# Kernel tuning notes

Measured on AMD Instinct MI355X. Metric: run time of the kernel, lower is better.

Reference implementation:

```python
import jax, jax.numpy as jnp
import numpy as np

B, T, N, E = 64, 500, 21, 210
IN_DIM, HID, OUT_DIM = 1, 128, 1


def gcn_norm(edge_index, edge_weight, num_nodes):
    # PyG gcn_norm: add self loops (weight 1), deg over target nodes, symmetric normalization.
    src, dst = edge_index[0], edge_index[1]
    loop = jnp.arange(num_nodes)
    src = jnp.concatenate([src, loop])
    dst = jnp.concatenate([dst, loop])
    ew = jnp.concatenate([edge_weight, jnp.ones((num_nodes,), edge_weight.dtype)])
    deg = jnp.zeros((num_nodes,), edge_weight.dtype).at[dst].add(ew)
    dinv = jnp.where(deg > 0, deg ** -0.5, 0.0)
    norm = dinv[src] * ew * dinv[dst]
    # Dense N x N (N=21, tiny) normalized adjacency; out[i] = sum_j A[i, j] x[j].
    return jnp.zeros((num_nodes, num_nodes), edge_weight.dtype).at[dst, src].add(norm)


def _forward(edge_index, x, edge_weight, Wz_1, bz_1, lzw_1, lzb_1, Wr_1, br_1, lrw_1, lrb_1, Wh_1, bh_1, lhw_1, lhb_1, Wz_2, bz_2, lzw_2, lzb_2, Wr_2, br_2, lrw_2, lrb_2, Wh_2, bh_2, lhw_2, lhb_2, cls_w, cls_b):
    A = gcn_norm(edge_index, edge_weight, N)

    def gcn(X, W, b):  # X: (B, N, F)
        return jnp.einsum("ij,bjf->bif", A, X @ W) + b

    def cell(X, H, Wz, bz, lzw, lzb, Wr, br, lrw, lrb, Wh, bh, lhw, lhb):
        Z = jax.nn.sigmoid(jnp.concatenate([gcn(X, Wz, bz), H], -1) @ lzw + lzb)
        R = jax.nn.sigmoid(jnp.concatenate([gcn(X, Wr, br), H], -1) @ lrw + lrb)
        Ht = jnp.tanh(jnp.concatenate([gcn(X, Wh, bh), H * R], -1) @ lhw + lhb)
        return Z * H + (1.0 - Z) * Ht

    def step(carry, x_t):  # x_t: (B, N)
        H1, H2 = carry
        X = x_t[..., None]  # (B, N, 1)
        H1 = cell(X, H1, Wz_1, bz_1, lzw_1, lzb_1, Wr_1, br_1, lrw_1, lrb_1, Wh_1, bh_1, lhw_1, lhb_1)
        H2 = cell(H1, H2, Wz_2, bz_2, lzw_2, lzb_2, Wr_2, br_2, lrw_2, lrb_2, Wh_2, bh_2, lhw_2, lhb_2)
        return (H1, H2), H2.mean(axis=1)  # mean over nodes -> (B, HID)

    H0 = jnp.zeros((x.shape[0], N, HID), x.dtype)
    _, outs = jax.lax.scan(step, (H0, H0), jnp.moveaxis(x, 1, 0))  # outs: (T, B, HID)
    seq_out = outs.mean(axis=0)  # mean over time (== mean over nodes then time in original)
    return seq_out @ cls_w + cls_b  # (B, OUT_DIM)


def setup_inputs():
    key = jax.random.key(0)
    ks = list(jax.random.split(key, 20))
    kit = iter(ks)

    def nrm(shape, scale=0.05):
        return jax.random.normal(next(kit), shape, jnp.float32) * scale

    inp = {}
    inp["x"] = jax.random.normal(next(kit), (B, T, N), jnp.float32)
    inp["edge_index"] = jax.random.randint(next(kit), (2, E), 0, N)
    inp["edge_weight"] = jax.random.uniform(next(kit), (E,), jnp.float32)
    for tag, in_dim in (("1", IN_DIM), ("2", HID)):
        for g in "zrh":
            inp[f"W{g}_{tag}"] = nrm((in_dim, HID))
            inp[f"b{g}_{tag}"] = jnp.zeros((HID,), jnp.float32)
            inp[f"l{g}w_{tag}"] = nrm((2 * HID, HID))
            inp[f"l{g}b_{tag}"] = jnp.zeros((HID,), jnp.float32)
    inp["cls_w"] = nrm((HID, OUT_DIM))
    inp["cls_b"] = jnp.zeros((OUT_DIM,), jnp.float32)
    return inp


def reference(x, edge_index, edge_weight, Wz_1, bz_1, lzw_1, lzb_1, Wr_1, br_1, lrw_1, lrb_1, Wh_1, bh_1, lhw_1, lhb_1, Wz_2, bz_2, lzw_2, lzb_2, Wr_2, br_2, lrw_2, lrb_2, Wh_2, bh_2, lhw_2, lhb_2, cls_w, cls_b):
    return _forward(edge_index, x, edge_weight, Wz_1, bz_1, lzw_1, lzb_1, Wr_1, br_1, lrw_1, lrb_1, Wh_1, bh_1, lhw_1, lhb_1, Wz_2, bz_2, lzw_2, lzb_2, Wr_2, br_2, lrw_2, lrb_2, Wh_2, bh_2, lhw_2, lhb_2, cls_w, cls_b)
```

## Files before the change

kernel.cpp:

```cpp
#include <hip/hip_runtime.h>
#include <hip/hip_bf16.h>


#define NN 21
#define NROW 24
#define HID 128
#define TSTEPS 500
#define EDGES 210
#define NTHREADS 512
#define RPT 6

#define WS_A     0
#define WS_VEC   1600
#define WS_LZR1  3200
#define WS_LH1   36000
#define WS_WE2   52400
#define WS_LZR2  101600
#define WS_LH2   134400

#define WAVE_SYNC() asm volatile("s_waitcnt lgkmcnt(0)" ::: "memory")

typedef float v2f __attribute__((ext_vector_type(2)));

__device__ __forceinline__ v2f lo2(float4 w) { v2f v = {w.x, w.y}; return v; }
__device__ __forceinline__ v2f hi2(float4 w) { v2f v = {w.z, w.w}; return v; }
__device__ __forceinline__ void pkf(v2f& acc, float s, v2f w) {
    v2f ss = {s, s};
    acc = __builtin_elementwise_fma(ss, w, acc);
}
__device__ __forceinline__ float sigmoidf(float v) {
    return 1.0f / (1.0f + expf(-v));
}

__global__ void build_A(const int* __restrict__ ei, const float* __restrict__ ew,
                        float* __restrict__ Aout) {
    __shared__ double deg[NN];
    __shared__ double dinv[NN];
    __shared__ double Asm[NN * NN];
    int t = threadIdx.x;
    for (int k = t; k < NN * NN; k += blockDim.x) Asm[k] = 0.0;
    if (t < NN) deg[t] = 1.0;
    __syncthreads();
    if (t == 0) {
        for (int e = 0; e < EDGES; e++) deg[ei[EDGES + e]] += (double)ew[e];
        for (int i = 0; i < NN; i++) dinv[i] = deg[i] > 0.0 ? 1.0 / sqrt(deg[i]) : 0.0;
        for (int e = 0; e < EDGES; e++) {
            int s = ei[e], d = ei[EDGES + e];
            Asm[d * NN + s] += dinv[s] * (double)ew[e] * dinv[d];
        }
        for (int i = 0; i < NN; i++) Asm[i * NN + i] += dinv[i] * dinv[i];
    }
    __syncthreads();
    for (int k = t; k < NROW * NN; k += blockDim.x)
        Aout[k] = (k < NN * NN) ? (float)Asm[k] : 0.0f;
}

__global__ void pack_bot(const float* __restrict__ w0, const float* __restrict__ w1,
                         float4* __restrict__ out, int ngate) {
    int t = blockIdx.x * blockDim.x + threadIdx.x;
    int per_c = ngate * 128;
    int total = 32 * per_c;
    if (t >= total) return;
    int c = t / per_c, rem = t - c * per_c;
    int gate = rem >> 7;
    int r2 = rem & 127;
    int k2 = r2 >> 6;
    int f0 = r2 & 63;
    int k = 4 * c + 2 * k2;
    const float* src = (gate == 0) ? w0 : w1;
    float4 v;
    v.x = src[(128 + k) * 128 + f0];
    v.y = src[(128 + k) * 128 + f0 + 64];
    v.z = src[(128 + k + 1) * 128 + f0];
    v.w = src[(128 + k + 1) * 128 + f0 + 64];
    out[t] = v;
}

__global__ void make_weff2(const float* __restrict__ Wz2, const float* __restrict__ Wr2,
                           const float* __restrict__ Wh2,
                           const float* __restrict__ lzw2, const float* __restrict__ lrw2,
                           const float* __restrict__ lhw2,
                           float4* __restrict__ out) {
    int t = blockIdx.x * blockDim.x + threadIdx.x;
    if (t >= 32 * 384) return;
    int c = t / 384, rem = t - c * 384;
    int g = rem >> 7;
    int r2 = rem & 127;
    int k2 = r2 >> 6;
    int f0 = r2 & 63;
    int k = 4 * c + 2 * k2;
    const float* W = (g == 0) ? Wz2 : (g == 1) ? Wr2 : Wh2;
    const float* L = (g == 0) ? lzw2 : (g == 1) ? lrw2 : lhw2;
    double a0 = 0, a1 = 0, a2 = 0, a3 = 0;
    for (int m = 0; m < 128; m++) {
        double w0 = (double)W[k * 128 + m];
        double w1 = (double)W[(k + 1) * 128 + m];
        a0 += w0 * (double)L[m * 128 + f0];
        a1 += w0 * (double)L[m * 128 + f0 + 64];
        a2 += w1 * (double)L[m * 128 + f0];
        a3 += w1 * (double)L[m * 128 + f0 + 64];
    }
    out[t] = make_float4((float)a0, (float)a1, (float)a2, (float)a3);
}

__global__ void make_vecs(const float* __restrict__ Wz1, const float* __restrict__ Wr1,
                          const float* __restrict__ Wh1,
                          const float* __restrict__ bz1, const float* __restrict__ br1,
                          const float* __restrict__ bh1,
                          const float* __restrict__ lzw1, const float* __restrict__ lrw1,
                          const float* __restrict__ lhw1,
                          const float* __restrict__ lzb1, const float* __restrict__ lrb1,
                          const float* __restrict__ lhb1,
                          const float* __restrict__ bz2, const float* __restrict__ br2,
                          const float* __restrict__ bh2,
                          const float* __restrict__ lzw2, const float* __restrict__ lrw2,
                          const float* __restrict__ lhw2,
                          const float* __restrict__ lzb2, const float* __restrict__ lrb2,
                          const float* __restrict__ lhb2,
                          float* __restrict__ out) {
    int t = blockIdx.x * blockDim.x + threadIdx.x;
    if (t >= 9 * 128) return;
    int v = t >> 7, f = t & 127;
    double acc = 0.0;
    if (v < 3) {
        const float* W = (v == 0) ? Wz1 : (v == 1) ? Wr1 : Wh1;
        const float* L = (v == 0) ? lzw1 : (v == 1) ? lrw1 : lhw1;
        for (int m = 0; m < 128; m++) acc += (double)W[m] * (double)L[m * 128 + f];
    } else if (v < 6) {
        int g = v - 3;
        const float* bb = (g == 0) ? bz1 : (g == 1) ? br1 : bh1;
        const float* L  = (g == 0) ? lzw1 : (g == 1) ? lrw1 : lhw1;
        const float* lb = (g == 0) ? lzb1 : (g == 1) ? lrb1 : lhb1;
        for (int m = 0; m < 128; m++) acc += (double)bb[m] * (double)L[m * 128 + f];
        acc += (double)lb[f];
    } else {
        int g = v - 6;
        const float* bb = (g == 0) ? bz2 : (g == 1) ? br2 : bh2;
        const float* L  = (g == 0) ? lzw2 : (g == 1) ? lrw2 : lhw2;
        const float* lb = (g == 0) ? lzb2 : (g == 1) ? lrb2 : lhb2;
        for (int m = 0; m < 128; m++) acc += (double)bb[m] * (double)L[m * 128 + f];
        acc += (double)lb[f];
    }
    out[t] = (float)acc;
}

__global__ __launch_bounds__(NTHREADS, 2) void tgcn_main(
    const float* __restrict__ x,
    const float* __restrict__ ws,
    const float* __restrict__ cls_w,
    const float* __restrict__ cls_b,
    float* __restrict__ out)
{
    const int b  = blockIdx.x;
    const int t  = threadIdx.x;
    const bool isA = (t < 256);
    const int lt = t & 255;
    const int f0 = lt & 63;
    const int f1 = f0 + 64;
    const int gw = __builtin_amdgcn_readfirstlane(lt >> 6);
    const int iA = gw * RPT;
    const int nreal = (iA + RPT <= NN) ? RPT : (NN - iA);

    __shared__ __align__(16) float sH1[2][NROW * HID];
    __shared__ __align__(16) float sH2[NROW * HID];
    __shared__ __align__(16) float sHR1[NROW * HID];
    __shared__ __align__(16) float sHR2[NROW * HID];
    __shared__ __align__(16) float sAH[NROW * HID];
    __shared__ float sA[NROW * NN];
    __shared__ float sax[2][NROW];
    __shared__ double sred[4][HID];

    const float*  vecs = ws + WS_VEC;
    const float4* Lzr1 = (const float4*)(ws + WS_LZR1);
    const float4* Lh1  = (const float4*)(ws + WS_LH1);
    const float4* We2  = (const float4*)(ws + WS_WE2);
    const float4* Lzr2 = (const float4*)(ws + WS_LZR2);
    const float4* Lh2  = (const float4*)(ws + WS_LH2);

    const float4* H2v  = (const float4*)sH2;
    const float4* HR1v = (const float4*)sHR1;
    const float4* HR2v = (const float4*)sHR2;
    const float4* AHv  = (const float4*)sAH;

    for (int k = t; k < 2 * NROW * HID; k += NTHREADS) ((float*)sH1)[k] = 0.0f;
    for (int k = t; k < NROW * HID; k += NTHREADS) sH2[k] = 0.0f;
    for (int k = t; k < NROW * NN; k += NTHREADS) sA[k] = ws[WS_A + k];

    const v2f wz1v = {vecs[f0],        vecs[f1]};
    const v2f wr1v = {vecs[128 + f0],  vecs[128 + f1]};
    const v2f wh1v = {vecs[256 + f0],  vecs[256 + f1]};
    const v2f cz1v = {vecs[384 + f0],  vecs[384 + f1]};
    const v2f cr1v = {vecs[512 + f0],  vecs[512 + f1]};
    const v2f ch1v = {vecs[640 + f0],  vecs[640 + f1]};
    const v2f cz2v = {vecs[768 + f0],  vecs[768 + f1]};
    const v2f cr2v = {vecs[896 + f0],  vecs[896 + f1]};
    const v2f ch2v = {vecs[1024 + f0], vecs[1024 + f1]};

    __syncthreads();

    const float* xb = x + (size_t)b * (TSTEPS * NN);
    if (t < NROW) {
        float a0s = 0.0f, a1s = 0.0f;
        for (int j = 0; j < NN; j++) {
            a0s = fmaf(sA[t * NN + j], xb[j], a0s);
            a1s = fmaf(sA[t * NN + j], xb[NN + j], a1s);
        }
        sax[0][t] = a0s;
        sax[1][t] = a1s;
    }
    __syncthreads();

    double oacc0 = 0.0, oacc1 = 0.0;

    auto layer1 = [&](int s) {
        const float* H1rd = sH1[(s + 1) & 1];
        float*       H1wr = sH1[s & 1];
        const float4* H1c = (const float4*)H1rd;
        float axp[RPT];
        #pragma unroll
        for (int r = 0; r < RPT; r++) axp[r] = sax[s & 1][iA + r];
        v2f az[RPT], ar[RPT];
        #pragma unroll
        for (int r = 0; r < RPT; r++) {
            az[r] = __builtin_elementwise_fma((v2f){axp[r], axp[r]}, wz1v, cz1v);
            ar[r] = __builtin_elementwise_fma((v2f){axp[r], axp[r]}, wr1v, cr1v);
        }
        #pragma unroll 2
        for (int c = 0; c < 32; ++c) {
            const float4 wz0 = Lzr1[c * 256 + f0];
            const float4 wz1 = Lzr1[c * 256 + 64 + f0];
            const float4 wr0 = Lzr1[c * 256 + 128 + f0];
            const float4 wr1 = Lzr1[c * 256 + 192 + f0];
            #pragma unroll
            for (int r = 0; r < RPT; r++) {
                const float4 h = H1c[(iA + r) * 32 + c];
                pkf(az[r], h.x, lo2(wz0)); pkf(az[r], h.y, hi2(wz0));
                pkf(az[r], h.z, lo2(wz1)); pkf(az[r], h.w, hi2(wz1));
                pkf(ar[r], h.x, lo2(wr0)); pkf(ar[r], h.y, hi2(wr0));
                pkf(ar[r], h.z, lo2(wr1)); pkf(ar[r], h.w, hi2(wr1));
            }
        }
        v2f zg[RPT], h1c[RPT];
        #pragma unroll
        for (int r = 0; r < RPT; r++) {
            zg[r].x = sigmoidf(az[r].x);
            zg[r].y = sigmoidf(az[r].y);
            const float r0 = sigmoidf(ar[r].x);
            const float r1 = sigmoidf(ar[r].y);
            h1c[r].x = H1rd[(iA + r) * HID + f0];
            h1c[r].y = H1rd[(iA + r) * HID + f1];
            sHR1[(iA + r) * HID + f0] = h1c[r].x * r0;
            sHR1[(iA + r) * HID + f1] = h1c[r].y * r1;
        }
        WAVE_SYNC();
        v2f ah[RPT];
        #pragma unroll
        for (int r = 0; r < RPT; r++)
            ah[r] = __builtin_elementwise_fma((v2f){axp[r], axp[r]}, wh1v, ch1v);
        #pragma unroll 2
        for (int c = 0; c < 32; ++c) {
            const float4 wh0 = Lh1[c * 128 + f0];
            const float4 wh1 = Lh1[c * 128 + 64 + f0];
            #pragma unroll
            for (int r = 0; r < RPT; r++) {
                const float4 q = HR1v[(iA + r) * 32 + c];
                pkf(ah[r], q.x, lo2(wh0)); pkf(ah[r], q.y, hi2(wh0));
                pkf(ah[r], q.z, lo2(wh1)); pkf(ah[r], q.w, hi2(wh1));
            }
        }
        #pragma unroll
        for (int r = 0; r < RPT; r++) {
            const float n0 = fmaf(zg[r].x, h1c[r].x, (1.0f - zg[r].x) * tanhf(ah[r].x));
            const float n1 = fmaf(zg[r].y, h1c[r].y, (1.0f - zg[r].y) * tanhf(ah[r].y));
            H1wr[(iA + r) * HID + f0] = n0;
            H1wr[(iA + r) * HID + f1] = n1;
        }
    };

    if (isA) layer1(0);
    __syncthreads();

    for (int k = 0; k < TSTEPS; k++) {
        if (isA) {
            if (k + 1 < TSTEPS) {
                layer1(k + 1);
                if (t < NROW && k + 2 < TSTEPS) {
                    const float* xt = xb + (size_t)(k + 2) * NN;
                    float a = 0.0f;
                    for (int j = 0; j < NN; j++) a = fmaf(sA[t * NN + j], xt[j], a);
                    sax[(k + 2) & 1][t] = a;
                }
            }
        } else {
            const float* H1rd = sH1[k & 1];
            v2f aa[RPT];
            #pragma unroll
            for (int r = 0; r < RPT; r++) aa[r] = (v2f){0.0f, 0.0f};
            #pragma unroll 3
            for (int j = 0; j < NN; j++) {
                const v2f hj = {H1rd[j * HID + f0], H1rd[j * HID + f1]};
                #pragma unroll
                for (int r = 0; r < RPT; r++) {
                    const float arj = sA[(iA + r) * NN + j];
                    acc_p3: ;
                    aa[r] = __builtin_elementwise_fma((v2f){arj, arj}, hj, aa[r]);
                }
            }
            #pragma unroll
            for (int r = 0; r < RPT; r++) {
                sAH[(iA + r) * HID + f0] = aa[r].x;
                sAH[(iA + r) * HID + f1] = aa[r].y;
            }
            WAVE_SYNC();
            v2f pz[RPT], pr[RPT], ph[RPT];
            #pragma unroll
            for (int r = 0; r < RPT; r++) { pz[r] = cz2v; pr[r] = cr2v; ph[r] = ch2v; }
            for (int c = 0; c < 32; ++c) {
                const float4 wz0 = We2[c * 384 + f0];
                const float4 wz1 = We2[c * 384 + 64 + f0];
                const float4 wr0 = We2[c * 384 + 128 + f0];
                const float4 wr1 = We2[c * 384 + 192 + f0];
                const float4 wh0 = We2[c * 384 + 256 + f0];
                const float4 wh1 = We2[c * 384 + 320 + f0];
                const float4 lz0 = Lzr2[c * 256 + f0];
                const float4 lz1 = Lzr2[c * 256 + 64 + f0];
                const float4 lr0 = Lzr2[c * 256 + 128 + f0];
                const float4 lr1 = Lzr2[c * 256 + 192 + f0];
                #pragma unroll
                for (int r = 0; r < RPT; r++) {
                    const float4 a = AHv[(iA + r) * 32 + c];
                    const float4 q = H2v[(iA + r) * 32 + c];
                    pkf(pz[r], a.x, lo2(wz0)); pkf(pz[r], a.y, hi2(wz0));
                    pkf(pz[r], a.z, lo2(wz1)); pkf(pz[r], a.w, hi2(wz1));
                    pkf(pz[r], q.x, lo2(lz0)); pkf(pz[r], q.y, hi2(lz0));
                    pkf(pz[r], q.z, lo2(lz1)); pkf(pz[r], q.w, hi2(lz1));
                    pkf(pr[r], a.x, lo2(wr0)); pkf(pr[r], a.y, hi2(wr0));
                    pkf(pr[r], a.z, lo2(wr1)); pkf(pr[r], a.w, hi2(wr1));
                    pkf(pr[r], q.x, lo2(lr0)); pkf(pr[r], q.y, hi2(lr0));
                    pkf(pr[r], q.z, lo2(lr1)); pkf(pr[r], q.w, hi2(lr1));
                    pkf(ph[r], a.x, lo2(wh0)); pkf(ph[r], a.y, hi2(wh0));
                    pkf(ph[r], a.z, lo2(wh1)); pkf(ph[r], a.w, hi2(wh1));
                }
            }
            v2f z2[RPT], h2c[RPT];
            #pragma unroll
            for (int r = 0; r < RPT; r++) {
                z2[r].x = sigmoidf(pz[r].x);
                z2[r].y = sigmoidf(pz[r].y);
                const float r20 = sigmoidf(pr[r].x);
                const float r21 = sigmoidf(pr[r].y);
                h2c[r].x = sH2[(iA + r) * HID + f0];
                h2c[r].y = sH2[(iA + r) * HID + f1];
                sHR2[(iA + r) * HID + f0] = h2c[r].x * r20;
                sHR2[(iA + r) * HID + f1] = h2c[r].y * r21;
            }
            WAVE_SYNC();
            #pragma unroll 2
            for (int c = 0; c < 32; ++c) {
                const float4 lh0 = Lh2[c * 128 + f0];
                const float4 lh1 = Lh2[c * 128 + 64 + f0];
                #pragma unroll
                for (int r = 0; r < RPT; r++) {
                    const float4 q = HR2v[(iA + r) * 32 + c];
                    pkf(ph[r], q.x, lo2(lh0)); pkf(ph[r], q.y, hi2(lh0));
                    pkf(ph[r], q.z, lo2(lh1)); pkf(ph[r], q.w, hi2(lh1));
                }
            }
            #pragma unroll
            for (int r = 0; r < RPT; r++) {
                const float m0 = fmaf(z2[r].x, h2c[r].x, (1.0f - z2[r].x) * tanhf(ph[r].x));
                const float m1 = fmaf(z2[r].y, h2c[r].y, (1.0f - z2[r].y) * tanhf(ph[r].y));
                sH2[(iA + r) * HID + f0] = m0;
                sH2[(iA + r) * HID + f1] = m1;
                if (r < nreal) {
                    oacc0 += (double)m0;
                    oacc1 += (double)m1;
                }
            }
        }
        __syncthreads();
    }

    if (!isA) {
        sred[gw][f0] = oacc0;
        sred[gw][f1] = oacc1;
    }
    __syncthreads();
    if (t < HID) {
        double s = 0.0;
        for (int gg = 0; gg < 4; gg++) s += sred[gg][t];
        sred[0][t] = (s / (double)(TSTEPS * NN)) * (double)cls_w[t];
    }
    __syncthreads();
    if (t < 64) {
        double v = ((double*)sred)[t] + ((double*)sred)[t + 64];
        for (int off = 32; off; off >>= 1) v += __shfl_down(v, off, 64);
        if (t == 0) out[b] = (float)(v + (double)cls_b[0]);
    }
}

extern "C" void kernel_launch(void* const* d_in, const int* in_sizes, int n_in,
                              void* d_out, int out_size, void* d_ws, size_t ws_size,
                              hipStream_t stream) {
    const float* x    = (const float*)d_in[0];
    const int*   ei   = (const int*)  d_in[1];
    const float* ew   = (const float*)d_in[2];
    const float* Wz1  = (const float*)d_in[3];
    const float* bz1  = (const float*)d_in[4];
    const float* lzw1 = (const float*)d_in[5];
    const float* lzb1 = (const float*)d_in[6];
    const float* Wr1  = (const float*)d_in[7];
    const float* br1  = (const float*)d_in[8];
    const float* lrw1 = (const float*)d_in[9];
    const float* lrb1 = (const float*)d_in[10];
    const float* Wh1  = (const float*)d_in[11];
    const float* bh1  = (const float*)d_in[12];
    const float* lhw1 = (const float*)d_in[13];
    const float* lhb1 = (const float*)d_in[14];
    const float* Wz2  = (const float*)d_in[15];
    const float* bz2  = (const float*)d_in[16];
    const float* lzw2 = (const float*)d_in[17];
    const float* lzb2 = (const float*)d_in[18];
    const float* Wr2  = (const float*)d_in[19];
    const float* br2  = (const float*)d_in[20];
    const float* lrw2 = (const float*)d_in[21];
    const float* lrb2 = (const float*)d_in[22];
    const float* Wh2  = (const float*)d_in[23];
    const float* bh2  = (const float*)d_in[24];
    const float* lhw2 = (const float*)d_in[25];
    const float* lhb2 = (const float*)d_in[26];
    const float* clsw = (const float*)d_in[27];
    const float* clsb = (const float*)d_in[28];

    float* ws   = (float*)d_ws;
    float* outp = (float*)d_out;

    build_A<<<1, 64, 0, stream>>>(ei, ew, ws + WS_A);
    pack_bot<<<32, 256, 0, stream>>>(lzw1, lrw1, (float4*)(ws + WS_LZR1), 2);
    pack_bot<<<16, 256, 0, stream>>>(lhw1, lhw1, (float4*)(ws + WS_LH1), 1);
    pack_bot<<<32, 256, 0, stream>>>(lzw2, lrw2, (float4*)(ws + WS_LZR2), 2);
    pack_bot<<<16, 256, 0, stream>>>(lhw2, lhw2, (float4*)(ws + WS_LH2), 1);
    make_weff2<<<48, 256, 0, stream>>>(Wz2, Wr2, Wh2, lzw2, lrw2, lhw2,
                                       (float4*)(ws + WS_WE2));
    make_vecs<<<5, 256, 0, stream>>>(Wz1, Wr1, Wh1, bz1, br1, bh1,
                                     lzw1, lrw1, lhw1, lzb1, lrb1, lhb1,
                                     bz2, br2, bh2, lzw2, lrw2, lhw2,
                                     lzb2, lrb2, lhb2, ws + WS_VEC);
    tgcn_main<<<64, NTHREADS, 0, stream>>>(x, ws, clsw, clsb, outp);
}
```

Baseline: 12.50 ms.

## Remap lanes across rows and columns, pad LDS rows, replace wave syncs with barriers

Each wave now owns a 16-column slice across all row blocks, not one row block across all 64 columns. The 16 lanes within a row group read weight float4s, so each global or L2 weight load is shared by fewer rows per wave but spread differently. The LDS row stride is padded to 132 floats to avoid bank conflicts. Because a wave's outputs are now read by other waves, the intra-wave lgkmcnt syncs are replaced by block-wide __syncthreads, and each step is split into three phases. Loop unroll pragmas are dropped. This adds two extra block barriers per timestep and changes register pressure.

```diff
diff --git a/kernel.cpp b/kernel.cpp
--- a/kernel.cpp
+++ b/kernel.cpp
@@ -9,6 +9,8 @@
 #define EDGES 210
 #define NTHREADS 512
 #define RPT 6
+#define RS 132
+#define RS4 33
 
 #define WS_A     0
 #define WS_VEC   1600
@@ -17,8 +19,6 @@
 #define WS_WE2   52400
 #define WS_LZR2  101600
 #define WS_LH2   134400
-
-#define WAVE_SYNC() asm volatile("s_waitcnt lgkmcnt(0)" ::: "memory")
 
 typedef float v2f __attribute__((ext_vector_type(2)));
 
@@ -151,21 +151,24 @@
     const float* __restrict__ cls_b,
     float* __restrict__ out)
 {
-    const int b  = blockIdx.x;
-    const int t  = threadIdx.x;
+    const int b    = blockIdx.x;
+    const int t    = threadIdx.x;
     const bool isA = (t < 256);
-    const int lt = t & 255;
-    const int f0 = lt & 63;
-    const int f1 = f0 + 64;
-    const int gw = __builtin_amdgcn_readfirstlane(lt >> 6);
-    const int iA = gw * RPT;
+    const int lt   = t & 255;
+    const int w    = __builtin_amdgcn_readfirstlane(lt >> 6);
+    const int lane = lt & 63;
+    const int cp   = lane & 15;
+    const int rb   = lane >> 4;
+    const int f0   = w * 16 + cp;
+    const int f1   = f0 + 64;
+    const int iA   = rb * RPT;
     const int nreal = (iA + RPT <= NN) ? RPT : (NN - iA);
 
-    __shared__ __align__(16) float sH1[2][NROW * HID];
-    __shared__ __align__(16) float sH2[NROW * HID];
-    __shared__ __align__(16) float sHR1[NROW * HID];
-    __shared__ __align__(16) float sHR2[NROW * HID];
-    __shared__ __align__(16) float sAH[NROW * HID];
+    __shared__ __align__(16) float sH1[2][NROW * RS];
+    __shared__ __align__(16) float sH2[NROW * RS];
+    __shared__ __align__(16) float sHR1[NROW * RS];
+    __shared__ __align__(16) float sHR2[NROW * RS];
+    __shared__ __align__(16) float sAH[NROW * RS];
     __shared__ float sA[NROW * NN];
     __shared__ float sax[2][NROW];
     __shared__ double sred[4][HID];
@@ -182,8 +185,8 @@
     const float4* HR2v = (const float4*)sHR2;
     const float4* AHv  = (const float4*)sAH;
 
-    for (int k = t; k < 2 * NROW * HID; k += NTHREADS) ((float*)sH1)[k] = 0.0f;
-    for (int k = t; k < NROW * HID; k += NTHREADS) sH2[k] = 0.0f;
+    for (int k = t; k < 2 * NROW * RS; k += NTHREADS) ((float*)sH1)[k] = 0.0f;
+    for (int k = t; k < NROW * RS; k += NTHREADS) sH2[k] = 0.0f;
     for (int k = t; k < NROW * NN; k += NTHREADS) sA[k] = ws[WS_A + k];
 
     const v2f wz1v = {vecs[f0],        vecs[f1]};
@@ -212,20 +215,21 @@
 
     double oacc0 = 0.0, oacc1 = 0.0;
 
-    auto layer1 = [&](int s) {
+    float axpA[RPT];
+    v2f   zgA[RPT], h1cA[RPT];
+    v2f   phB[RPT], z2B[RPT], h2cB[RPT];
+
+    auto a_p1 = [&](int s) {
         const float* H1rd = sH1[(s + 1) & 1];
-        float*       H1wr = sH1[s & 1];
         const float4* H1c = (const float4*)H1rd;
-        float axp[RPT];
         #pragma unroll
-        for (int r = 0; r < RPT; r++) axp[r] = sax[s & 1][iA + r];
+        for (int r = 0; r < RPT; r++) axpA[r] = sax[s & 1][iA + r];
         v2f az[RPT], ar[RPT];
         #pragma unroll
         for (int r = 0; r < RPT; r++) {
-            az[r] = __builtin_elementwise_fma((v2f){axp[r], axp[r]}, wz1v, cz1v);
-            ar[r] = __builtin_elementwise_fma((v2f){axp[r], axp[r]}, wr1v, cr1v);
-        }
-        #pragma unroll 2
+            az[r] = __builtin_elementwise_fma((v2f){axpA[r], axpA[r]}, wz1v, cz1v);
+            ar[r] = __builtin_elementwise_fma((v2f){axpA[r], axpA[r]}, wr1v, cr1v);
+        }
         for (int c = 0; c < 32; ++c) {
             const float4 wz0 = Lzr1[c * 256 + f0];
             const float4 wz1 = Lzr1[c * 256 + 64 + f0];
@@ -233,88 +237,86 @@
             const float4 wr1 = Lzr1[c * 256 + 192 + f0];
             #pragma unroll
             for (int r = 0; r < RPT; r++) {
-                const float4 h = H1c[(iA + r) * 32 + c];
+                const float4 h = H1c[(iA + r) * RS4 + c];
                 pkf(az[r], h.x, lo2(wz0)); pkf(az[r], h.y, hi2(wz0));
                 pkf(az[r], h.z, lo2(wz1)); pkf(az[r], h.w, hi2(wz1));
                 pkf(ar[r], h.x, lo2(wr0)); pkf(ar[r], h.y, hi2(wr0));
                 pkf(ar[r], h.z, lo2(wr1)); pkf(ar[r], h.w, hi2(wr1));
             }
         }
-        v2f zg[RPT], h1c[RPT];
         #pragma unroll
         for (int r = 0; r < RPT; r++) {
-            zg[r].x = sigmoidf(az[r].x);
-            zg[r].y = sigmoidf(az[r].y);
+            zgA[r].x = sigmoidf(az[r].x);
+            zgA[r].y = sigmoidf(az[r].y);
             const float r0 = sigmoidf(ar[r].x);
             const float r1 = sigmoidf(ar[r].y);
-            h1c[r].x = H1rd[(iA + r) * HID + f0];
-            h1c[r].y = H1rd[(iA + r) * HID + f1];
-            sHR1[(iA + r) * HID + f0] = h1c[r].x * r0;
-            sHR1[(iA + r) * HID + f1] = h1c[r].y * r1;
-        }
-        WAVE_SYNC();
+            h1cA[r].x = H1rd[(iA + r) * RS + f0];
+            h1cA[r].y = H1rd[(iA + r) * RS + f1];
+            sHR1[(iA + r) * RS + f0] = h1cA[r].x * r0;
+            sHR1[(iA + r) * RS + f1] = h1cA[r].y * r1;
+        }
+    };
+    auto a_p2 = [&](int s) {
+        float* H1wr = sH1[s & 1];
         v2f ah[RPT];
         #pragma unroll
         for (int r = 0; r < RPT; r++)
-            ah[r] = __builtin_elementwise_fma((v2f){axp[r], axp[r]}, wh1v, ch1v);
-        #pragma unroll 2
+            ah[r] = __builtin_elementwise_fma((v2f){axpA[r], axpA[r]}, wh1v, ch1v);
         for (int c = 0; c < 32; ++c) {
             const float4 wh0 = Lh1[c * 128 + f0];
             const float4 wh1 = Lh1[c * 128 + 64 + f0];
             #pragma unroll
             for (int r = 0; r < RPT; r++) {
-                const float4 q = HR1v[(iA + r) * 32 + c];
+                const float4 q = HR1v[(iA + r) * RS4 + c];
                 pkf(ah[r], q.x, lo2(wh0)); pkf(ah[r], q.y, hi2(wh0));
                 pkf(ah[r], q.z, lo2(wh1)); pkf(ah[r], q.w, hi2(wh1));
             }
         }
         #pragma unroll
         for (int r = 0; r < RPT; r++) {
-            const float n0 = fmaf(zg[r].x, h1c[r].x, (1.0f - zg[r].x) * tanhf(ah[r].x));
-            const float n1 = fmaf(zg[r].y, h1c[r].y, (1.0f - zg[r].y) * tanhf(ah[r].y));
-            H1wr[(iA + r) * HID + f0] = n0;
-            H1wr[(iA + r) * HID + f1] = n1;
+            const float n0 = fmaf(zgA[r].x, h1cA[r].x, (1.0f - zgA[r].x) * tanhf(ah[r].x));
+            const float n1 = fmaf(zgA[r].y, h1cA[r].y, (1.0f - zgA[r].y) * tanhf(ah[r].y));
+            H1wr[(iA + r) * RS + f0] = n0;
+            H1wr[(iA + r) * RS + f1] = n1;
         }
     };
 
-    if (isA) layer1(0);
+    if (isA) a_p1(0);
+    __syncthreads();
+    if (isA) a_p2(0);
     __syncthreads();
 
     for (int k = 0; k < TSTEPS; k++) {
+        const bool doA = (k + 1 < TSTEPS);
         if (isA) {
-            if (k + 1 < TSTEPS) {
-                layer1(k + 1);
-                if (t < NROW && k + 2 < TSTEPS) {
-                    const float* xt = xb + (size_t)(k + 2) * NN;
-                    float a = 0.0f;
-                    for (int j = 0; j < NN; j++) a = fmaf(sA[t * NN + j], xt[j], a);
-                    sax[(k + 2) & 1][t] = a;
-                }
-            }
+            if (doA) a_p1(k + 1);
         } else {
             const float* H1rd = sH1[k & 1];
             v2f aa[RPT];
             #pragma unroll
             for (int r = 0; r < RPT; r++) aa[r] = (v2f){0.0f, 0.0f};
-            #pragma unroll 3
             for (int j = 0; j < NN; j++) {
-                const v2f hj = {H1rd[j * HID + f0], H1rd[j * HID + f1]};
+                const v2f hj = {H1rd[j * RS + f0], H1rd[j * RS + f1]};
                 #pragma unroll
                 for (int r = 0; r < RPT; r++) {
                     const float arj = sA[(iA + r) * NN + j];
-                    acc_p3: ;
                     aa[r] = __builtin_elementwise_fma((v2f){arj, arj}, hj, aa[r]);
                 }
             }
             #pragma unroll
             for (int r = 0; r < RPT; r++) {
-                sAH[(iA + r) * HID + f0] = aa[r].x;
-                sAH[(iA + r) * HID + f1] = aa[r].y;
-            }
-            WAVE_SYNC();
-            v2f pz[RPT], pr[RPT], ph[RPT];
-            #pragma unroll
-            for (int r = 0; r < RPT; r++) { pz[r] = cz2v; pr[r] = cr2v; ph[r] = ch2v; }
+                sAH[(iA + r) * RS + f0] = aa[r].x;
+                sAH[(iA + r) * RS + f1] = aa[r].y;
+            }
+        }
+        __syncthreads();
+
+        if (isA) {
+            if (doA) a_p2(k + 1);
+        } else {
+            v2f pz[RPT], pr[RPT];
+            #pragma unroll
+            for (int r = 0; r < RPT; r++) { pz[r] = cz2v; pr[r] = cr2v; phB[r] = ch2v; }
             for (int c = 0; c < 32; ++c) {
                 const float4 wz0 = We2[c * 384 + f0];
                 const float4 wz1 = We2[c * 384 + 64 + f0];
@@ -328,8 +330,8 @@
                 const float4 lr1 = Lzr2[c * 256 + 192 + f0];
                 #pragma unroll
                 for (int r = 0; r < RPT; r++) {
-                    const float4 a = AHv[(iA + r) * 32 + c];
-                    const float4 q = H2v[(iA + r) * 32 + c];
+                    const float4 a = AHv[(iA + r) * RS4 + c];
+                    const float4 q = H2v[(iA + r) * RS4 + c];
                     pkf(pz[r], a.x, lo2(wz0)); pkf(pz[r], a.y, hi2(wz0));
                     pkf(pz[r], a.z, lo2(wz1)); pkf(pz[r], a.w, hi2(wz1));
                     pkf(pz[r], q.x, lo2(lz0)); pkf(pz[r], q.y, hi2(lz0));
@@ -338,40 +340,48 @@
                     pkf(pr[r], a.z, lo2(wr1)); pkf(pr[r], a.w, hi2(wr1));
                     pkf(pr[r], q.x, lo2(lr0)); pkf(pr[r], q.y, hi2(lr0));
                     pkf(pr[r], q.z, lo2(lr1)); pkf(pr[r], q.w, hi2(lr1));
-                    pkf(ph[r], a.x, lo2(wh0)); pkf(ph[r], a.y, hi2(wh0));
-                    pkf(ph[r], a.z, lo2(wh1)); pkf(ph[r], a.w, hi2(wh1));
+                    pkf(phB[r], a.x, lo2(wh0)); pkf(phB[r], a.y, hi2(wh0));
+                    pkf(phB[r], a.z, lo2(wh1)); pkf(phB[r], a.w, hi2(wh1));
                 }
             }
-            v2f z2[RPT], h2c[RPT];
             #pragma unroll
             for (int r = 0; r < RPT; r++) {
-                z2[r].x = sigmoidf(pz[r].x);
-                z2[r].y = sigmoidf(pz[r].y);
+                z2B[r].x = sigmoidf(pz[r].x);
+                z2B[r].y = sigmoidf(pz[r].y);
                 const float r20 = sigmoidf(pr[r].x);
                 const float r21 = sigmoidf(pr[r].y);
-                h2c[r].x = sH2[(iA + r) * HID + f0];
-                h2c[r].y = sH2[(iA + r) * HID + f1];
-                sHR2[(iA + r) * HID + f0] = h2c[r].x * r20;
-                sHR2[(iA + r) * HID + f1] = h2c[r].y * r21;
-            }
-            WAVE_SYNC();
-            #pragma unroll 2
+                h2cB[r].x = sH2[(iA + r) * RS + f0];
+                h2cB[r].y = sH2[(iA + r) * RS + f1];
+                sHR2[(iA + r) * RS + f0] = h2cB[r].x * r20;
+                sHR2[(iA + r) * RS + f1] = h2cB[r].y * r21;
+            }
+        }
+        __syncthreads();
+
+        if (isA) {
+            if (t < NROW && k + 2 < TSTEPS) {
+                const float* xt = xb + (size_t)(k + 2) * NN;
+                float a = 0.0f;
+                for (int j = 0; j < NN; j++) a = fmaf(sA[t * NN + j], xt[j], a);
+                sax[(k + 2) & 1][t] = a;
+            }
+        } else {
             for (int c = 0; c < 32; ++c) {
                 const float4 lh0 = Lh2[c * 128 + f0];
                 const float4 lh1 = Lh2[c * 128 + 64 + f0];
                 #pragma unroll
                 for (int r = 0; r < RPT; r++) {
-                    const float4 q = HR2v[(iA + r) * 32 + c];
-                    pkf(ph[r], q.x, lo2(lh0)); pkf(ph[r], q.y, hi2(lh0));
-                    pkf(ph[r], q.z, lo2(lh1)); pkf(ph[r], q.w, hi2(lh1));
+                    const float4 q = HR2v[(iA + r) * RS4 + c];
+                    pkf(phB[r], q.x, lo2(lh0)); pkf(phB[r], q.y, hi2(lh0));
+                    pkf(phB[r], q.z, lo2(lh1)); pkf(phB[r], q.w, hi2(lh1));
                 }
             }
             #pragma unroll
             for (int r = 0; r < RPT; r++) {
-                const float m0 = fmaf(z2[r].x, h2c[r].x, (1.0f - z2[r].x) * tanhf(ph[r].x));
-                const float m1 = fmaf(z2[r].y, h2c[r].y, (1.0f - z2[r].y) * tanhf(ph[r].y));
-                sH2[(iA + r) * HID + f0] = m0;
-                sH2[(iA + r) * HID + f1] = m1;
+                const float m0 = fmaf(z2B[r].x, h2cB[r].x, (1.0f - z2B[r].x) * tanhf(phB[r].x));
+                const float m1 = fmaf(z2B[r].y, h2cB[r].y, (1.0f - z2B[r].y) * tanhf(phB[r].y));
+                sH2[(iA + r) * RS + f0] = m0;
+                sH2[(iA + r) * RS + f1] = m1;
                 if (r < nreal) {
                     oacc0 += (double)m0;
                     oacc1 += (double)m1;
@@ -382,8 +392,8 @@
     }
 
     if (!isA) {
-        sred[gw][f0] = oacc0;
-        sred[gw][f1] = oacc1;
+        sred[rb][f0] = oacc0;
+        sred[rb][f1] = oacc1;
     }
     __syncthreads();
     if (t < HID) {
```

Result: slower. 16.76 ms (+34.1%).

## Move hidden-state and A·H operand reads from LDS to global memory buffers

Applied to the files above, without the earlier changes.

Moves the H1 read buffer, the A·H1 product and H2 out of shared memory into per-block global workspace, read through float4 global loads. Each thread keeps its own previous hidden values in registers, so the gate update no longer reloads them. The aim is to relieve LDS bandwidth and bank pressure by sending matmul operand reads through the vector cache. It removes a wave-level sync after the A·H write and drops several unroll pragmas. The cost is global-memory latency on the critical recurrence and a dependence on the cache staying coherent for data written and then read within the same block.

```diff
diff --git a/kernel.cpp b/kernel.cpp
--- a/kernel.cpp
+++ b/kernel.cpp
@@ -17,6 +17,9 @@
 #define WS_WE2   52400
 #define WS_LZR2  101600
 #define WS_LH2   134400
+#define WS_H1G   150784
+#define WS_AHG   544000
+#define WS_H2G   740608
 
 #define WAVE_SYNC() asm volatile("s_waitcnt lgkmcnt(0)" ::: "memory")
 
@@ -147,6 +150,9 @@
 __global__ __launch_bounds__(NTHREADS, 2) void tgcn_main(
     const float* __restrict__ x,
     const float* __restrict__ ws,
+    float* __restrict__ h1g,
+    float* __restrict__ ahg,
+    float* __restrict__ h2g,
     const float* __restrict__ cls_w,
     const float* __restrict__ cls_b,
     float* __restrict__ out)
@@ -161,11 +167,13 @@
     const int iA = gw * RPT;
     const int nreal = (iA + RPT <= NN) ? RPT : (NN - iA);
 
+    float* h1gb = h1g + (size_t)b * 6144;
+    float* ahgb = ahg + (size_t)b * 3072;
+    float* h2gb = h2g + (size_t)b * 3072;
+
     __shared__ __align__(16) float sH1[2][NROW * HID];
-    __shared__ __align__(16) float sH2[NROW * HID];
     __shared__ __align__(16) float sHR1[NROW * HID];
     __shared__ __align__(16) float sHR2[NROW * HID];
-    __shared__ __align__(16) float sAH[NROW * HID];
     __shared__ float sA[NROW * NN];
     __shared__ float sax[2][NROW];
     __shared__ double sred[4][HID];
@@ -177,13 +185,12 @@
     const float4* Lzr2 = (const float4*)(ws + WS_LZR2);
     const float4* Lh2  = (const float4*)(ws + WS_LH2);
 
-    const float4* H2v  = (const float4*)sH2;
     const float4* HR1v = (const float4*)sHR1;
     const float4* HR2v = (const float4*)sHR2;
-    const float4* AHv  = (const float4*)sAH;
 
     for (int k = t; k < 2 * NROW * HID; k += NTHREADS) ((float*)sH1)[k] = 0.0f;
-    for (int k = t; k < NROW * HID; k += NTHREADS) sH2[k] = 0.0f;
+    for (int k = t; k < 6144; k += NTHREADS) h1gb[k] = 0.0f;
+    for (int k = t; k < 3072; k += NTHREADS) h2gb[k] = 0.0f;
     for (int k = t; k < NROW * NN; k += NTHREADS) sA[k] = ws[WS_A + k];
 
     const v2f wz1v = {vecs[f0],        vecs[f1]};
@@ -212,10 +219,15 @@
 
     double oacc0 = 0.0, oacc1 = 0.0;
 
+    v2f h1keep[RPT];
+    v2f h2keep[RPT];
+    #pragma unroll
+    for (int r = 0; r < RPT; r++) { h1keep[r] = (v2f){0.f, 0.f}; h2keep[r] = (v2f){0.f, 0.f}; }
+
     auto layer1 = [&](int s) {
-        const float* H1rd = sH1[(s + 1) & 1];
-        float*       H1wr = sH1[s & 1];
-        const float4* H1c = (const float4*)H1rd;
+        const float4* gH1 = (const float4*)(h1gb + ((s + 1) & 1) * 3072);
+        float* H1wrL = sH1[s & 1];
+        float* H1wrG = h1gb + (s & 1) * 3072;
         float axp[RPT];
         #pragma unroll
         for (int r = 0; r < RPT; r++) axp[r] = sax[s & 1][iA + r];
@@ -225,7 +237,6 @@
             az[r] = __builtin_elementwise_fma((v2f){axp[r], axp[r]}, wz1v, cz1v);
             ar[r] = __builtin_elementwise_fma((v2f){axp[r], axp[r]}, wr1v, cr1v);
         }
-        #pragma unroll 2
         for (int c = 0; c < 32; ++c) {
             const float4 wz0 = Lzr1[c * 256 + f0];
             const float4 wz1 = Lzr1[c * 256 + 64 + f0];
@@ -233,7 +244,7 @@
             const float4 wr1 = Lzr1[c * 256 + 192 + f0];
             #pragma unroll
             for (int r = 0; r < RPT; r++) {
-                const float4 h = H1c[(iA + r) * 32 + c];
+                const float4 h = gH1[(iA + r) * 32 + c];
                 pkf(az[r], h.x, lo2(wz0)); pkf(az[r], h.y, hi2(wz0));
                 pkf(az[r], h.z, lo2(wz1)); pkf(az[r], h.w, hi2(wz1));
                 pkf(ar[r], h.x, lo2(wr0)); pkf(ar[r], h.y, hi2(wr0));
@@ -247,8 +258,7 @@
             zg[r].y = sigmoidf(az[r].y);
             const float r0 = sigmoidf(ar[r].x);
             const float r1 = sigmoidf(ar[r].y);
-            h1c[r].x = H1rd[(iA + r) * HID + f0];
-            h1c[r].y = H1rd[(iA + r) * HID + f1];
+            h1c[r] = h1keep[r];
             sHR1[(iA + r) * HID + f0] = h1c[r].x * r0;
             sHR1[(iA + r) * HID + f1] = h1c[r].y * r1;
         }
@@ -257,7 +267,6 @@
         #pragma unroll
         for (int r = 0; r < RPT; r++)
             ah[r] = __builtin_elementwise_fma((v2f){axp[r], axp[r]}, wh1v, ch1v);
-        #pragma unroll 2
         for (int c = 0; c < 32; ++c) {
             const float4 wh0 = Lh1[c * 128 + f0];
             const float4 wh1 = Lh1[c * 128 + 64 + f0];
@@ -272,8 +281,11 @@
         for (int r = 0; r < RPT; r++) {
             const float n0 = fmaf(zg[r].x, h1c[r].x, (1.0f - zg[r].x) * tanhf(ah[r].x));
             const float n1 = fmaf(zg[r].y, h1c[r].y, (1.0f - zg[r].y) * tanhf(ah[r].y));
-            H1wr[(iA + r) * HID + f0] = n0;
-            H1wr[(iA + r) * HID + f1] = n1;
+            H1wrL[(iA + r) * HID + f0] = n0;
+            H1wrL[(iA + r) * HID + f1] = n1;
+            H1wrG[(iA + r) * HID + f0] = n0;
+            H1wrG[(iA + r) * HID + f1] = n1;
+            h1keep[r] = (v2f){n0, n1};
         }
     };
 
@@ -296,22 +308,21 @@
             v2f aa[RPT];
             #pragma unroll
             for (int r = 0; r < RPT; r++) aa[r] = (v2f){0.0f, 0.0f};
-            #pragma unroll 3
             for (int j = 0; j < NN; j++) {
                 const v2f hj = {H1rd[j * HID + f0], H1rd[j * HID + f1]};
                 #pragma unroll
                 for (int r = 0; r < RPT; r++) {
                     const float arj = sA[(iA + r) * NN + j];
-                    acc_p3: ;
                     aa[r] = __builtin_elementwise_fma((v2f){arj, arj}, hj, aa[r]);
                 }
             }
             #pragma unroll
             for (int r = 0; r < RPT; r++) {
-                sAH[(iA + r) * HID + f0] = aa[r].x;
-                sAH[(iA + r) * HID + f1] = aa[r].y;
-            }
-            WAVE_SYNC();
+                ahgb[(iA + r) * HID + f0] = aa[r].x;
+                ahgb[(iA + r) * HID + f1] = aa[r].y;
+            }
+            const float4* gAH = (const float4*)ahgb;
+            const float4* gH2 = (const float4*)h2gb;
             v2f pz[RPT], pr[RPT], ph[RPT];
             #pragma unroll
             for (int r = 0; r < RPT; r++) { pz[r] = cz2v; pr[r] = cr2v; ph[r] = ch2v; }
@@ -328,8 +339,8 @@
                 const float4 lr1 = Lzr2[c * 256 + 192 + f0];
                 #pragma unroll
                 for (int r = 0; r < RPT; r++) {
-                    const float4 a = AHv[(iA + r) * 32 + c];
-                    const float4 q = H2v[(iA + r) * 32 + c];
+                    const float4 a = gAH[(iA + r) * 32 + c];
+                    const float4 q = gH2[(iA + r) * 32 + c];
                     pkf(pz[r], a.x, lo2(wz0)); pkf(pz[r], a.y, hi2(wz0));
                     pkf(pz[r], a.z, lo2(wz1)); pkf(pz[r], a.w, hi2(wz1));
                     pkf(pz[r], q.x, lo2(lz0)); pkf(pz[r], q.y, hi2(lz0));
@@ -349,13 +360,11 @@
                 z2[r].y = sigmoidf(pz[r].y);
                 const float r20 = sigmoidf(pr[r].x);
                 const float r21 = sigmoidf(pr[r].y);
-                h2c[r].x = sH2[(iA + r) * HID + f0];
-                h2c[r].y = sH2[(iA + r) * HID + f1];
+                h2c[r] = h2keep[r];
                 sHR2[(iA + r) * HID + f0] = h2c[r].x * r20;
                 sHR2[(iA + r) * HID + f1] = h2c[r].y * r21;
             }
             WAVE_SYNC();
-            #pragma unroll 2
             for (int c = 0; c < 32; ++c) {
                 const float4 lh0 = Lh2[c * 128 + f0];
                 const float4 lh1 = Lh2[c * 128 + 64 + f0];
@@ -370,8 +379,9 @@
             for (int r = 0; r < RPT; r++) {
                 const float m0 = fmaf(z2[r].x, h2c[r].x, (1.0f - z2[r].x) * tanhf(ph[r].x));
                 const float m1 = fmaf(z2[r].y, h2c[r].y, (1.0f - z2[r].y) * tanhf(ph[r].y));
-                sH2[(iA + r) * HID + f0] = m0;
-                sH2[(iA + r) * HID + f1] = m1;
+                h2gb[(iA + r) * HID + f0] = m0;
+                h2gb[(iA + r) * HID + f1] = m1;
+                h2keep[r] = (v2f){m0, m1};
                 if (r < nreal) {
                     oacc0 += (double)m0;
                     oacc1 += (double)m1;
@@ -446,5 +456,7 @@
                                      lzw1, lrw1, lhw1, lzb1, lrb1, lhb1,
                                      bz2, br2, bh2, lzw2, lrw2, lhw2,
                                      lzb2, lrb2, lhb2, ws + WS_VEC);
-    tgcn_main<<<64, NTHREADS, 0, stream>>>(x, ws, clsw, clsb, outp);
-}
+    tgcn_main<<<64, NTHREADS, 0, stream>>>(x, ws,
+                                           ws + WS_H1G, ws + WS_AHG, ws + WS_H2G,
+                                           clsw, clsb, outp);
+}
```

New measurement: 21.82 ms. +74.5%, slower.
